# Kernel tuning notes

Measured on AMD Instinct MI355X. Metric: run time of the kernel, lower is better.

The kernel has to match this reference:

```python
import jax, jax.numpy as jnp
import numpy as np

ITERS = 10
EPS = 1e-6
TEMPERATURE = 1.0


def setup_inputs() -> dict:
    key = jax.random.key(0)
    S, E = 524288, 64
    logits = jax.random.normal(key, (S, E), dtype=jnp.float32)
    return {"logits": logits, "top_k": 2}


def reference(logits, top_k):
    s, e = logits.shape
    scores = (logits / TEMPERATURE).astype(jnp.float32)
    scores = scores - jnp.max(scores, axis=-1, keepdims=True)
    q = jnp.exp(scores)
    col_target = float(s) / float(max(e, 1))

    def body(q, _):
        q = q / (jnp.sum(q, axis=1, keepdims=True) + EPS)
        q = q / (jnp.sum(q, axis=0, keepdims=True) + EPS) * col_target
        return q, None

    q, _ = jax.lax.scan(body, q, None, length=ITERS)
    q = q / (jnp.sum(q, axis=1, keepdims=True) + EPS)
    vals, idx = jax.lax.top_k(q, top_k)
    w = vals / (jnp.sum(vals, axis=-1, keepdims=True) + EPS)
    return idx.astype(jnp.int64), w.astype(logits.dtype)
```

## Files before the change

### kernel.cpp

```cpp
#include <hip/hip_runtime.h>
#include <math.h>

#define EPS 1e-6f
#define NE 64
#define TPB 1024
#define WPB 16
#define NBLK 256
#define NWAVES (NBLK * WPB)
#define ITERS 10
#define PF 4

template <int ctrl>
__device__ __forceinline__ float dppf(float x) {
    return __int_as_float(__builtin_amdgcn_update_dpp(
        0, __float_as_int(x), ctrl, 0xf, 0xf, true));
}
template <int ctrl>
__device__ __forceinline__ int dppi(int x) {
    return __builtin_amdgcn_update_dpp(0, x, ctrl, 0xf, 0xf, true);
}

__device__ __forceinline__ float group16_sum(float v) {
    v += dppf<0xB1>(v);
    v += dppf<0x4E>(v);
    v += dppf<0x141>(v);
    v += dppf<0x140>(v);
    return v;
}

#define ARGMAX_STEP(CTRL)                                      \
    {                                                          \
        float ov = dppf<CTRL>(v);                              \
        int oi = dppi<CTRL>(i);                                \
        if (ov > v || (ov == v && oi < i)) { v = ov; i = oi; } \
    }

__device__ __forceinline__ void group16_argmax(float& v, int& i) {
    ARGMAX_STEP(0xB1)
    ARGMAX_STEP(0x4E)
    ARGMAX_STEP(0x141)
    ARGMAX_STEP(0x140)
}

template <bool FIRST>
__global__ __launch_bounds__(TPB) void sink_pass(
    const float4* __restrict__ logits4, float* __restrict__ r,
    float* __restrict__ c, float* __restrict__ Pblk,
    unsigned* __restrict__ counters, int nquads, float col_target, int it) {
    const int tid = threadIdx.x;
    const int lane = tid & 63;
    const int wib = tid >> 6;
    const int g = lane >> 4;
    const int h = lane & 15;
    const int qpw = nquads / NWAVES;
    const int qbase = (blockIdx.x * WPB + wib) * qpw;

    float4 c4;
    if (FIRST) c4 = make_float4(1.f, 1.f, 1.f, 1.f);
    else       c4 = ((const float4*)c)[h];

    const float4* lp = logits4 + (size_t)qbase * 64 + lane;

    float4 buf[PF];
    float rbuf[PF];
#pragma unroll
    for (int p = 0; p < PF; ++p) buf[p] = lp[(size_t)p * 64];
    if (!FIRST) {
#pragma unroll
        for (int p = 0; p < PF; ++p) rbuf[p] = r[(qbase + p) * 4 + g];
    }

    float4 pacc = {0.f, 0.f, 0.f, 0.f};
    const int nb = qpw / PF;
    for (int b = 0; b < nb; ++b) {
        float4 cur[PF];
        float rcur[PF];
#pragma unroll
        for (int p = 0; p < PF; ++p) {
            cur[p] = buf[p];
            if (!FIRST) rcur[p] = rbuf[p];
        }
        if (b + 1 < nb) {
            const float4* np = lp + (size_t)(b + 1) * PF * 64;
#pragma unroll
            for (int p = 0; p < PF; ++p) buf[p] = np[(size_t)p * 64];
            if (!FIRST) {
#pragma unroll
                for (int p = 0; p < PF; ++p)
                    rbuf[p] = r[(qbase + (b + 1) * PF + p) * 4 + g];
            }
        }
#pragma unroll
        for (int p = 0; p < PF; ++p) {
            float4 q;
            q.x = __expf(cur[p].x); q.y = __expf(cur[p].y);
            q.z = __expf(cur[p].z); q.w = __expf(cur[p].w);
            float s = q.x * c4.x + q.y * c4.y + q.z * c4.z + q.w * c4.w;
            s = group16_sum(s);
            float rold = FIRST ? 1.0f : rcur[p];
            float rnew = rold / (rold * s + EPS);
            int row = (qbase + b * PF + p) * 4 + g;
            if (h == 0) r[row] = rnew;
            pacc.x += q.x * rnew; pacc.y += q.y * rnew;
            pacc.z += q.z * rnew; pacc.w += q.w * rnew;
        }
    }

    __shared__ float4 plds[WPB][64];
    __shared__ int lastflag;
    plds[wib][lane] = pacc;
    __syncthreads();
    if (tid < NE) {
        int j = tid, hh = j >> 2, kk = j & 3;
        float t = 0.f;
#pragma unroll
        for (int w = 0; w < WPB; ++w)
#pragma unroll
            for (int gg = 0; gg < 4; ++gg)
                t += ((const float*)&plds[w][gg * 16 + hh])[kk];
        Pblk[blockIdx.x * NE + j] = t;
        __threadfence();
    }
    __syncthreads();
    if (tid == 0) {
        unsigned old = atomicAdd(&counters[it], 1u);
        lastflag = (old == (unsigned)(NBLK - 1));
    }
    __syncthreads();

    if (lastflag) {
        __threadfence();
        float* s_red = (float*)plds;
        const int j = tid & 63;
        const int chunk = tid >> 6;
        float t = 0.f;
        int b0 = chunk * (NBLK / 16);
        for (int b = b0; b < b0 + NBLK / 16; ++b) t += Pblk[b * NE + j];
        __syncthreads();
        s_red[chunk * NE + j] = t;
        __syncthreads();
        if (tid < NE) {
            float P = 0.f;
#pragma unroll
            for (int k = 0; k < 16; ++k) P += s_red[k * NE + tid];
            float cj = FIRST ? 1.0f : c[tid];
            c[tid] = cj * col_target / (cj * P + EPS);
            __threadfence();
        }
    }
}

__global__ __launch_bounds__(TPB) void sink_final(
    const float4* __restrict__ logits4, const float* __restrict__ r,
    const float* __restrict__ c, float2* __restrict__ oidx,
    float2* __restrict__ ow, int nquads) {
    const int tid = threadIdx.x;
    const int lane = tid & 63;
    const int wib = tid >> 6;
    const int g = lane >> 4;
    const int h = lane & 15;
    const int base_col = h * 4;
    const int qpw = nquads / NWAVES;
    const int qbase = (blockIdx.x * WPB + wib) * qpw;

    const float4 c4 = ((const float4*)c)[h];
    const float4* lp = logits4 + (size_t)qbase * 64 + lane;

    float4 buf[PF];
    float rbuf[PF];
#pragma unroll
    for (int p = 0; p < PF; ++p) buf[p] = lp[(size_t)p * 64];
#pragma unroll
    for (int p = 0; p < PF; ++p) rbuf[p] = r[(qbase + p) * 4 + g];

    const int nb = qpw / PF;
    for (int b = 0; b < nb; ++b) {
        float4 cur[PF];
        float rcur[PF];
#pragma unroll
        for (int p = 0; p < PF; ++p) { cur[p] = buf[p]; rcur[p] = rbuf[p]; }
        if (b + 1 < nb) {
            const float4* np = lp + (size_t)(b + 1) * PF * 64;
#pragma unroll
            for (int p = 0; p < PF; ++p) buf[p] = np[(size_t)p * 64];
#pragma unroll
            for (int p = 0; p < PF; ++p)
                rbuf[p] = r[(qbase + (b + 1) * PF + p) * 4 + g];
        }
#pragma unroll
        for (int p = 0; p < PF; ++p) {
            float4 u;
            u.x = __expf(cur[p].x) * c4.x; u.y = __expf(cur[p].y) * c4.y;
            u.z = __expf(cur[p].z) * c4.z; u.w = __expf(cur[p].w) * c4.w;
            float s = group16_sum(u.x + u.y + u.z + u.w);
            float rold = rcur[p];
            float rnew = rold / (rold * s + EPS);
            float4 val;
            val.x = u.x * rnew; val.y = u.y * rnew;
            val.z = u.z * rnew; val.w = u.w * rnew;

            float v = val.x; int i = base_col;
            if (val.y > v) { v = val.y; i = base_col + 1; }
            if (val.z > v) { v = val.z; i = base_col + 2; }
            if (val.w > v) { v = val.w; i = base_col + 3; }
            group16_argmax(v, i);
            float v1 = v; int i1 = i;

            float4 mv;
            mv.x = (i1 == base_col)     ? -INFINITY : val.x;
            mv.y = (i1 == base_col + 1) ? -INFINITY : val.y;
            mv.z = (i1 == base_col + 2) ? -INFINITY : val.z;
            mv.w = (i1 == base_col + 3) ? -INFINITY : val.w;
            v = mv.x; i = base_col;
            if (mv.y > v) { v = mv.y; i = base_col + 1; }
            if (mv.z > v) { v = mv.z; i = base_col + 2; }
            if (mv.w > v) { v = mv.w; i = base_col + 3; }
            group16_argmax(v, i);
            float v2 = v; int i2 = i;

            if (h == 0) {
                int row = (qbase + b * PF + p) * 4 + g;
                float wsum = v1 + v2 + EPS;
                oidx[row] = make_float2((float)i1, (float)i2);
                ow[row] = make_float2(v1 / wsum, v2 / wsum);
            }
        }
    }
}

extern "C" void kernel_launch(void* const* d_in, const int* in_sizes, int n_in,
                              void* d_out, int out_size, void* d_ws, size_t ws_size,
                              hipStream_t stream) {
    const float* logits = (const float*)d_in[0];
    const int S = in_sizes[0] / NE;
    const int nquads = S / 4;
    const float col_target = (float)S / (float)NE;

    float* r = (float*)d_ws;
    float* c = r + S;
    float* Pblk = c + NE;
    unsigned* counters = (unsigned*)(Pblk + NBLK * NE);

    float* out = (float*)d_out;
    float2* oidx = (float2*)out;
    float2* ow = (float2*)(out + (size_t)2 * S);

    const float4* l4 = (const float4*)logits;

    hipMemsetAsync(counters, 0, ITERS * sizeof(unsigned), stream);
    sink_pass<true><<<NBLK, TPB, 0, stream>>>(l4, r, c, Pblk, counters,
                                              nquads, col_target, 0);
    for (int it = 1; it < ITERS; ++it)
        sink_pass<false><<<NBLK, TPB, 0, stream>>>(l4, r, c, Pblk, counters,
                                                   nquads, col_target, it);
    sink_final<<<NBLK, TPB, 0, stream>>>(l4, r, c, oidx, ow, nquads);
}
```

Measured before the change: 557.3 us.

## Fuse all Sinkhorn passes into one persistent kernel with grid barriers

Replaces the eleven launches (ten iteration passes plus final top-k) with one persistent kernel that synchronises all blocks through an atomic counter grid barrier between iterations. Row scale factors now stay in LDS instead of global memory, and column factors are recomputed redundantly by every block. Column partials are double-buffered in global memory. This removes launch gaps and the per-pass global r traffic, but relies on all 256 blocks being co-resident; if they are not, the spin barrier deadlocks.

After: 1.751 ms. +214.2%, slower.

```diff
diff --git a/kernel.cpp b/kernel.cpp
--- a/kernel.cpp
+++ b/kernel.cpp
@@ -42,11 +42,17 @@
     ARGMAX_STEP(0x140)
 }
 
-template <bool FIRST>
-__global__ __launch_bounds__(TPB) void sink_pass(
-    const float4* __restrict__ logits4, float* __restrict__ r,
-    float* __restrict__ c, float* __restrict__ Pblk,
-    unsigned* __restrict__ counters, int nquads, float col_target, int it) {
+__global__ __launch_bounds__(TPB, 4) void sink_fused(
+    const float4* __restrict__ logits4,
+    float* __restrict__ Pblk,
+    unsigned* __restrict__ counters,
+    float2* __restrict__ oidx, float2* __restrict__ ow,
+    int nquads, float col_target) {
+    __shared__ float4 plds[WPB][64];
+    __shared__ float s_red[16][NE];
+    __shared__ float r_lds[WPB * 128];
+    __shared__ float4 c_lds4[NE / 4];
+
     const int tid = threadIdx.x;
     const int lane = tid & 63;
     const int wib = tid >> 6;
@@ -54,175 +60,151 @@
     const int h = lane & 15;
     const int qpw = nquads / NWAVES;
     const int qbase = (blockIdx.x * WPB + wib) * qpw;
-
-    float4 c4;
-    if (FIRST) c4 = make_float4(1.f, 1.f, 1.f, 1.f);
-    else       c4 = ((const float4*)c)[h];
-
     const float4* lp = logits4 + (size_t)qbase * 64 + lane;
-
-    float4 buf[PF];
-    float rbuf[PF];
-#pragma unroll
-    for (int p = 0; p < PF; ++p) buf[p] = lp[(size_t)p * 64];
-    if (!FIRST) {
-#pragma unroll
-        for (int p = 0; p < PF; ++p) rbuf[p] = r[(qbase + p) * 4 + g];
-    }
-
-    float4 pacc = {0.f, 0.f, 0.f, 0.f};
     const int nb = qpw / PF;
-    for (int b = 0; b < nb; ++b) {
-        float4 cur[PF];
-        float rcur[PF];
-#pragma unroll
-        for (int p = 0; p < PF; ++p) {
-            cur[p] = buf[p];
-            if (!FIRST) rcur[p] = rbuf[p];
-        }
-        if (b + 1 < nb) {
-            const float4* np = lp + (size_t)(b + 1) * PF * 64;
-#pragma unroll
-            for (int p = 0; p < PF; ++p) buf[p] = np[(size_t)p * 64];
-            if (!FIRST) {
-#pragma unroll
-                for (int p = 0; p < PF; ++p)
-                    rbuf[p] = r[(qbase + (b + 1) * PF + p) * 4 + g];
-            }
-        }
-#pragma unroll
-        for (int p = 0; p < PF; ++p) {
-            float4 q;
-            q.x = __expf(cur[p].x); q.y = __expf(cur[p].y);
-            q.z = __expf(cur[p].z); q.w = __expf(cur[p].w);
-            float s = q.x * c4.x + q.y * c4.y + q.z * c4.z + q.w * c4.w;
-            s = group16_sum(s);
-            float rold = FIRST ? 1.0f : rcur[p];
-            float rnew = rold / (rold * s + EPS);
-            int row = (qbase + b * PF + p) * 4 + g;
-            if (h == 0) r[row] = rnew;
-            pacc.x += q.x * rnew; pacc.y += q.y * rnew;
-            pacc.z += q.z * rnew; pacc.w += q.w * rnew;
-        }
-    }
-
-    __shared__ float4 plds[WPB][64];
-    __shared__ int lastflag;
-    plds[wib][lane] = pacc;
+    const int lrow0 = wib * 128 + g;
+
+    if (tid < NE / 4) c_lds4[tid] = make_float4(1.f, 1.f, 1.f, 1.f);
     __syncthreads();
-    if (tid < NE) {
-        int j = tid, hh = j >> 2, kk = j & 3;
-        float t = 0.f;
-#pragma unroll
-        for (int w = 0; w < WPB; ++w)
-#pragma unroll
-            for (int gg = 0; gg < 4; ++gg)
-                t += ((const float*)&plds[w][gg * 16 + hh])[kk];
-        Pblk[blockIdx.x * NE + j] = t;
+
+    for (int it = 0; it < ITERS; ++it) {
+        const float4 c4 = c_lds4[h];
+        float* Pcur = Pblk + (size_t)(it & 1) * NBLK * NE;
+
+        float4 buf[PF];
+#pragma unroll
+        for (int p = 0; p < PF; ++p) buf[p] = lp[(size_t)p * 64];
+
+        float4 pacc = {0.f, 0.f, 0.f, 0.f};
+        for (int b = 0; b < nb; ++b) {
+            float4 cur[PF];
+#pragma unroll
+            for (int p = 0; p < PF; ++p) cur[p] = buf[p];
+            if (b + 1 < nb) {
+                const float4* np = lp + (size_t)(b + 1) * PF * 64;
+#pragma unroll
+                for (int p = 0; p < PF; ++p) buf[p] = np[(size_t)p * 64];
+            }
+#pragma unroll
+            for (int p = 0; p < PF; ++p) {
+                float4 q;
+                q.x = __expf(cur[p].x); q.y = __expf(cur[p].y);
+                q.z = __expf(cur[p].z); q.w = __expf(cur[p].w);
+                float s = q.x * c4.x + q.y * c4.y + q.z * c4.z + q.w * c4.w;
+                s = group16_sum(s);
+                const int lrow = lrow0 + (b * PF + p) * 4;
+                float rold = (it == 0) ? 1.0f : r_lds[lrow];
+                float rnew = rold / (rold * s + EPS);
+                if (h == 0) r_lds[lrow] = rnew;
+                pacc.x += q.x * rnew; pacc.y += q.y * rnew;
+                pacc.z += q.z * rnew; pacc.w += q.w * rnew;
+            }
+        }
+
+        plds[wib][lane] = pacc;
+        __syncthreads();
+        if (tid < NE) {
+            const int hh = tid >> 2, kk = tid & 3;
+            float t = 0.f;
+#pragma unroll
+            for (int w = 0; w < WPB; ++w)
+#pragma unroll
+                for (int gg = 0; gg < 4; ++gg)
+                    t += ((const float*)&plds[w][gg * 16 + hh])[kk];
+            __hip_atomic_store(&Pcur[blockIdx.x * NE + tid], t,
+                               __ATOMIC_RELAXED, __HIP_MEMORY_SCOPE_AGENT);
+        }
+        __syncthreads();
+
         __threadfence();
-    }
-    __syncthreads();
-    if (tid == 0) {
-        unsigned old = atomicAdd(&counters[it], 1u);
-        lastflag = (old == (unsigned)(NBLK - 1));
-    }
-    __syncthreads();
-
-    if (lastflag) {
+        if (tid == 0) {
+            __hip_atomic_fetch_add(&counters[it], 1u, __ATOMIC_ACQ_REL,
+                                   __HIP_MEMORY_SCOPE_AGENT);
+            while (__hip_atomic_load(&counters[it], __ATOMIC_ACQUIRE,
+                                     __HIP_MEMORY_SCOPE_AGENT) < (unsigned)NBLK)
+                __builtin_amdgcn_s_sleep(8);
+        }
+        __syncthreads();
         __threadfence();
-        float* s_red = (float*)plds;
-        const int j = tid & 63;
-        const int chunk = tid >> 6;
-        float t = 0.f;
-        int b0 = chunk * (NBLK / 16);
-        for (int b = b0; b < b0 + NBLK / 16; ++b) t += Pblk[b * NE + j];
-        __syncthreads();
-        s_red[chunk * NE + j] = t;
+
+        {
+            const int col = tid & 63;
+            const int chunk = tid >> 6;
+            const int b0 = chunk * (NBLK / 16);
+            float t = 0.f;
+#pragma unroll
+            for (int b2 = 0; b2 < NBLK / 16; ++b2)
+                t += __hip_atomic_load(&Pcur[(b0 + b2) * NE + col],
+                                       __ATOMIC_RELAXED,
+                                       __HIP_MEMORY_SCOPE_AGENT);
+            s_red[chunk][col] = t;
+        }
         __syncthreads();
         if (tid < NE) {
             float P = 0.f;
 #pragma unroll
-            for (int k = 0; k < 16; ++k) P += s_red[k * NE + tid];
-            float cj = FIRST ? 1.0f : c[tid];
-            c[tid] = cj * col_target / (cj * P + EPS);
-            __threadfence();
-        }
+            for (int k = 0; k < 16; ++k) P += s_red[k][tid];
+            float cj = ((float*)c_lds4)[tid];
+            ((float*)c_lds4)[tid] = cj * col_target / (cj * P + EPS);
+        }
+        __syncthreads();
     }
-}
-
-__global__ __launch_bounds__(TPB) void sink_final(
-    const float4* __restrict__ logits4, const float* __restrict__ r,
-    const float* __restrict__ c, float2* __restrict__ oidx,
-    float2* __restrict__ ow, int nquads) {
-    const int tid = threadIdx.x;
-    const int lane = tid & 63;
-    const int wib = tid >> 6;
-    const int g = lane >> 4;
-    const int h = lane & 15;
-    const int base_col = h * 4;
-    const int qpw = nquads / NWAVES;
-    const int qbase = (blockIdx.x * WPB + wib) * qpw;
-
-    const float4 c4 = ((const float4*)c)[h];
-    const float4* lp = logits4 + (size_t)qbase * 64 + lane;
-
-    float4 buf[PF];
-    float rbuf[PF];
-#pragma unroll
-    for (int p = 0; p < PF; ++p) buf[p] = lp[(size_t)p * 64];
-#pragma unroll
-    for (int p = 0; p < PF; ++p) rbuf[p] = r[(qbase + p) * 4 + g];
-
-    const int nb = qpw / PF;
-    for (int b = 0; b < nb; ++b) {
-        float4 cur[PF];
-        float rcur[PF];
-#pragma unroll
-        for (int p = 0; p < PF; ++p) { cur[p] = buf[p]; rcur[p] = rbuf[p]; }
-        if (b + 1 < nb) {
-            const float4* np = lp + (size_t)(b + 1) * PF * 64;
-#pragma unroll
-            for (int p = 0; p < PF; ++p) buf[p] = np[(size_t)p * 64];
-#pragma unroll
-            for (int p = 0; p < PF; ++p)
-                rbuf[p] = r[(qbase + (b + 1) * PF + p) * 4 + g];
-        }
-#pragma unroll
-        for (int p = 0; p < PF; ++p) {
-            float4 u;
-            u.x = __expf(cur[p].x) * c4.x; u.y = __expf(cur[p].y) * c4.y;
-            u.z = __expf(cur[p].z) * c4.z; u.w = __expf(cur[p].w) * c4.w;
-            float s = group16_sum(u.x + u.y + u.z + u.w);
-            float rold = rcur[p];
-            float rnew = rold / (rold * s + EPS);
-            float4 val;
-            val.x = u.x * rnew; val.y = u.y * rnew;
-            val.z = u.z * rnew; val.w = u.w * rnew;
-
-            float v = val.x; int i = base_col;
-            if (val.y > v) { v = val.y; i = base_col + 1; }
-            if (val.z > v) { v = val.z; i = base_col + 2; }
-            if (val.w > v) { v = val.w; i = base_col + 3; }
-            group16_argmax(v, i);
-            float v1 = v; int i1 = i;
-
-            float4 mv;
-            mv.x = (i1 == base_col)     ? -INFINITY : val.x;
-            mv.y = (i1 == base_col + 1) ? -INFINITY : val.y;
-            mv.z = (i1 == base_col + 2) ? -INFINITY : val.z;
-            mv.w = (i1 == base_col + 3) ? -INFINITY : val.w;
-            v = mv.x; i = base_col;
-            if (mv.y > v) { v = mv.y; i = base_col + 1; }
-            if (mv.z > v) { v = mv.z; i = base_col + 2; }
-            if (mv.w > v) { v = mv.w; i = base_col + 3; }
-            group16_argmax(v, i);
-            float v2 = v; int i2 = i;
-
-            if (h == 0) {
-                int row = (qbase + b * PF + p) * 4 + g;
-                float wsum = v1 + v2 + EPS;
-                oidx[row] = make_float2((float)i1, (float)i2);
-                ow[row] = make_float2(v1 / wsum, v2 / wsum);
+
+    {
+        const float4 c4 = c_lds4[h];
+        const int base_col = h * 4;
+
+        float4 buf[PF];
+#pragma unroll
+        for (int p = 0; p < PF; ++p) buf[p] = lp[(size_t)p * 64];
+
+        for (int b = 0; b < nb; ++b) {
+            float4 cur[PF];
+#pragma unroll
+            for (int p = 0; p < PF; ++p) cur[p] = buf[p];
+            if (b + 1 < nb) {
+                const float4* np = lp + (size_t)(b + 1) * PF * 64;
+#pragma unroll
+                for (int p = 0; p < PF; ++p) buf[p] = np[(size_t)p * 64];
+            }
+#pragma unroll
+            for (int p = 0; p < PF; ++p) {
+                float4 u;
+                u.x = __expf(cur[p].x) * c4.x; u.y = __expf(cur[p].y) * c4.y;
+                u.z = __expf(cur[p].z) * c4.z; u.w = __expf(cur[p].w) * c4.w;
+                float s = group16_sum(u.x + u.y + u.z + u.w);
+                const int lrow = lrow0 + (b * PF + p) * 4;
+                float rold = r_lds[lrow];
+                float rnew = rold / (rold * s + EPS);
+                float4 val;
+                val.x = u.x * rnew; val.y = u.y * rnew;
+                val.z = u.z * rnew; val.w = u.w * rnew;
+
+                float v = val.x; int i = base_col;
+                if (val.y > v) { v = val.y; i = base_col + 1; }
+                if (val.z > v) { v = val.z; i = base_col + 2; }
+                if (val.w > v) { v = val.w; i = base_col + 3; }
+                group16_argmax(v, i);
+                float v1 = v; int i1 = i;
+
+                float4 mv;
+                mv.x = (i1 == base_col)     ? -INFINITY : val.x;
+                mv.y = (i1 == base_col + 1) ? -INFINITY : val.y;
+                mv.z = (i1 == base_col + 2) ? -INFINITY : val.z;
+                mv.w = (i1 == base_col + 3) ? -INFINITY : val.w;
+                v = mv.x; i = base_col;
+                if (mv.y > v) { v = mv.y; i = base_col + 1; }
+                if (mv.z > v) { v = mv.z; i = base_col + 2; }
+                if (mv.w > v) { v = mv.w; i = base_col + 3; }
+                group16_argmax(v, i);
+                float v2 = v; int i2 = i;
+
+                if (h == 0) {
+                    int row = (qbase + b * PF + p) * 4 + g;
+                    float wsum = v1 + v2 + EPS;
+                    oidx[row] = make_float2((float)i1, (float)i2);
+                    ow[row] = make_float2(v1 / wsum, v2 / wsum);
+                }
             }
         }
     }
@@ -236,22 +218,14 @@
     const int nquads = S / 4;
     const float col_target = (float)S / (float)NE;
 
-    float* r = (float*)d_ws;
-    float* c = r + S;
-    float* Pblk = c + NE;
-    unsigned* counters = (unsigned*)(Pblk + NBLK * NE);
+    float* Pblk = (float*)d_ws;
+    unsigned* counters = (unsigned*)(Pblk + 2 * NBLK * NE);
 
     float* out = (float*)d_out;
     float2* oidx = (float2*)out;
     float2* ow = (float2*)(out + (size_t)2 * S);
 
-    const float4* l4 = (const float4*)logits;
-
     hipMemsetAsync(counters, 0, ITERS * sizeof(unsigned), stream);
-    sink_pass<true><<<NBLK, TPB, 0, stream>>>(l4, r, c, Pblk, counters,
-                                              nquads, col_target, 0);
-    for (int it = 1; it < ITERS; ++it)
-        sink_pass<false><<<NBLK, TPB, 0, stream>>>(l4, r, c, Pblk, counters,
-                                                   nquads, col_target, it);
-    sink_final<<<NBLK, TPB, 0, stream>>>(l4, r, c, oidx, ow, nquads);
-}
+    sink_fused<<<NBLK, TPB, 0, stream>>>((const float4*)logits, Pblk, counters,
+                                         oidx, ow, nquads, col_target);
+}
```
